# Optimization experiments

Hardware: AMD Instinct MI355X
Metric: run time of the kernel (lower is better)

Reference implementation:

```python
import jax, jax.numpy as jnp
import numpy as np

TOP_K = 10  # hard-coded k=10 in the original tf.nn.top_k call


def setup_inputs() -> dict:
    key = jax.random.key(0)
    k1, k2 = jax.random.split(key)
    x = jax.random.normal(k1, (32768, 128), dtype=jnp.float32)
    cluster_centers = jax.random.normal(k2, (512, 128), dtype=jnp.float32)
    return {"x": x, "cluster_centers": cluster_centers}


def reference(x, cluster_centers):
    # (mathematically identical to tf.norm(x[:, None, :] - centers, axis=-1)
    #  without materializing the [N, K, D] difference tensor).
    x2 = jnp.sum(x * x, axis=-1, keepdims=True)            # [N, 1]
    c2 = jnp.sum(cluster_centers * cluster_centers, -1)    # [K]
    d2 = x2 - 2.0 * (x @ cluster_centers.T) + c2           # [N, K]
    distances = jnp.sqrt(jnp.maximum(d2, 0.0))
    # top-k smallest distances -> cluster indices (values in [0, K))
    _, indices = jax.lax.top_k(-distances, TOP_K)          # [N, 10] int32
    # Faithful to the original: gather POINTS x at these cluster indices
    closest_points = x[indices]                            # [N, 10, D]
    return closest_points.reshape(1, -1, x.shape[-1])      # [1, N*10, D]
```

## Files before the change

kernel.cpp:

```cpp
#include <hip/hip_runtime.h>
#include <stdint.h>

#define NPTS 32768
#define NCEN 512
#define DIM  128
#define TOPK 10

#define BM 128
#define BN 128
#define LDT 132

__global__ __launch_bounds__(256) void np_rownorm(const float* __restrict__ src,
                                                  float* __restrict__ dst, int nrows) {
  const int t = threadIdx.x;
  const int lane = t & 63;
  const int wv = t >> 6;
  const int g = lane >> 3;
  const int j = lane & 7;
  const int row = blockIdx.x * 32 + wv * 8 + g;
  if (row >= nrows) return;
  const float* p = src + (size_t)row * DIM;

  float v = p[j];
  float r = __fmul_rn(v, v);
#pragma unroll
  for (int b = 1; b < 16; ++b) {
    v = p[8 * b + j];
    r = __fadd_rn(r, __fmul_rn(v, v));
  }
  r = __fadd_rn(r, __shfl_xor(r, 1, 64));
  r = __fadd_rn(r, __shfl_xor(r, 2, 64));
  r = __fadd_rn(r, __shfl_xor(r, 4, 64));
  if (j == 0) dst[row] = r;
}

__global__ __launch_bounds__(256) void dist_kernel(const float* __restrict__ x,
                                                   const float* __restrict__ cen,
                                                   const float* __restrict__ x2,
                                                   const float* __restrict__ c2,
                                                   float* __restrict__ dist) {
  __shared__ float xT[DIM][LDT];
  __shared__ float cT[DIM][LDT];

  const int t  = threadIdx.x;
  const int pb = blockIdx.y * BM;
  const int cb = blockIdx.x * BN;

  {
    const int p  = t & 127;
    const int kb = (t >> 7) * 64;
    const float4* srcx = (const float4*)&x[(size_t)(pb + p) * DIM + kb];
    const float4* srcc = (const float4*)&cen[(size_t)(cb + p) * DIM + kb];
#pragma unroll
    for (int i = 0; i < 16; ++i) {
      float4 v = srcx[i];
      int k = kb + i * 4;
      xT[k + 0][p] = v.x; xT[k + 1][p] = v.y; xT[k + 2][p] = v.z; xT[k + 3][p] = v.w;
    }
#pragma unroll
    for (int i = 0; i < 16; ++i) {
      float4 v = srcc[i];
      int k = kb + i * 4;
      cT[k + 0][p] = v.x; cT[k + 1][p] = v.y; cT[k + 2][p] = v.z; cT[k + 3][p] = v.w;
    }
  }
  __syncthreads();

  const int wid  = t >> 6;
  const int lane = t & 63;
  const int wr = wid >> 1, wc = wid & 1;
  const int r = lane & 7, c = lane >> 3;
  const int px = wr * 64 + 4 * r;
  const int cx = wc * 64 + 4 * c;

  float acc[8][8];
#pragma unroll
  for (int i = 0; i < 8; ++i)
#pragma unroll
    for (int j = 0; j < 8; ++j) acc[i][j] = 0.f;

#pragma unroll 4
  for (int k = 0; k < DIM; ++k) {
    float4 xa = *(const float4*)&xT[k][px];
    float4 xb = *(const float4*)&xT[k][px + 32];
    float4 ca = *(const float4*)&cT[k][cx];
    float4 cbv = *(const float4*)&cT[k][cx + 32];
    float xv[8] = {xa.x, xa.y, xa.z, xa.w, xb.x, xb.y, xb.z, xb.w};
    float cv[8] = {ca.x, ca.y, ca.z, ca.w, cbv.x, cbv.y, cbv.z, cbv.w};
#pragma unroll
    for (int i = 0; i < 8; ++i)
#pragma unroll
      for (int j = 0; j < 8; ++j)
        acc[i][j] = __fmaf_rn(xv[i], cv[j], acc[i][j]);
  }

#pragma unroll
  for (int i = 0; i < 8; ++i) {
    const int pt = px + (i & 3) + (i >> 2) * 32;
    const int p  = pb + pt;
    const float xx = x2[p];
#pragma unroll
    for (int jq = 0; jq < 2; ++jq) {
      const int cg = cb + cx + jq * 32;
      float4 cc = *(const float4*)&c2[cg];
      float t0 = __fmaf_rn(-2.f, acc[i][jq * 4 + 0], xx);
      float t1 = __fmaf_rn(-2.f, acc[i][jq * 4 + 1], xx);
      float t2 = __fmaf_rn(-2.f, acc[i][jq * 4 + 2], xx);
      float t3 = __fmaf_rn(-2.f, acc[i][jq * 4 + 3], xx);
      float4 o;
      o.x = sqrtf(fmaxf(__fadd_rn(t0, cc.x), 0.f));
      o.y = sqrtf(fmaxf(__fadd_rn(t1, cc.y), 0.f));
      o.z = sqrtf(fmaxf(__fadd_rn(t2, cc.z), 0.f));
      o.w = sqrtf(fmaxf(__fadd_rn(t3, cc.w), 0.f));
      *(float4*)&dist[(size_t)p * NCEN + cg] = o;
    }
  }
}

__global__ __launch_bounds__(256) void topk_gather_kernel(const float* __restrict__ dist,
                                                          const float* __restrict__ x,
                                                          float* __restrict__ out) {
  const int p    = blockIdx.x * 4 + (threadIdx.x >> 6);
  const int lane = threadIdx.x & 63;

  const float4* dp = (const float4*)(dist + (size_t)p * NCEN);
  float4 va = dp[lane];
  float4 vb = dp[lane + 64];

  unsigned long long key[8];
  {
    const unsigned ca = 4u * lane, cb = 256u + 4u * lane;
    key[0] = ((unsigned long long)__float_as_uint(va.x) << 32) | (ca + 0);
    key[1] = ((unsigned long long)__float_as_uint(va.y) << 32) | (ca + 1);
    key[2] = ((unsigned long long)__float_as_uint(va.z) << 32) | (ca + 2);
    key[3] = ((unsigned long long)__float_as_uint(va.w) << 32) | (ca + 3);
    key[4] = ((unsigned long long)__float_as_uint(vb.x) << 32) | (cb + 0);
    key[5] = ((unsigned long long)__float_as_uint(vb.y) << 32) | (cb + 1);
    key[6] = ((unsigned long long)__float_as_uint(vb.z) << 32) | (cb + 2);
    key[7] = ((unsigned long long)__float_as_uint(vb.w) << 32) | (cb + 3);
  }

  float* op = out + (size_t)p * TOPK * DIM;

#pragma unroll
  for (int t = 0; t < TOPK; ++t) {
    unsigned long long m = key[0];
#pragma unroll
    for (int s = 1; s < 8; ++s) m = (key[s] < m) ? key[s] : m;
#pragma unroll
    for (int off = 32; off > 0; off >>= 1) {
      unsigned long long o = __shfl_xor(m, off, 64);
      m = (o < m) ? o : m;
    }
#pragma unroll
    for (int s = 0; s < 8; ++s)
      if (key[s] == m) key[s] = ~0ull;

    const int idx = (int)(m & 0x1ffull);
    float2 v = *(const float2*)&x[(size_t)idx * DIM + 2 * lane];
    *(float2*)&op[(size_t)t * DIM + 2 * lane] = v;
  }
}

extern "C" void kernel_launch(void* const* d_in, const int* in_sizes, int n_in,
                              void* d_out, int out_size, void* d_ws, size_t ws_size,
                              hipStream_t stream) {
  const float* x   = (const float*)d_in[0];
  const float* cen = (const float*)d_in[1];
  float* out = (float*)d_out;

  float* c2   = (float*)d_ws;
  float* x2   = (float*)((char*)d_ws + 4096);
  float* dist = (float*)((char*)d_ws + 4096 + 131072);

  np_rownorm<<<NCEN / 32, 256, 0, stream>>>(cen, c2, NCEN);
  np_rownorm<<<NPTS / 32, 256, 0, stream>>>(x, x2, NPTS);
  dist_kernel<<<dim3(NCEN / BN, NPTS / BM), 256, 0, stream>>>(x, cen, x2, c2, dist);
  topk_gather_kernel<<<NPTS / 4, 256, 0, stream>>>(dist, x, out);
}
```

Baseline: 143.3 us.

## Tile the K dimension of the distance GEMM to shrink shared memory

The distance kernel now walks the 128-wide feature dimension in chunks of 32 instead of staging the whole tile at once. This cuts shared memory per block from about 135KB to about 34KB, and a launch bound asking for 4 blocks per multiprocessor is added so more blocks can be resident. The cost is four load/sync phases per block with no double buffering. The launch bound also caps registers for the 64-element accumulator, which could cause spills.

```diff
diff --git a/kernel.cpp b/kernel.cpp
--- a/kernel.cpp
+++ b/kernel.cpp
@@ -8,6 +8,7 @@
 
 #define BM 128
 #define BN 128
+#define KSTEP 32
 #define LDT 132
 
 __global__ __launch_bounds__(256) void np_rownorm(const float* __restrict__ src,
@@ -34,37 +35,20 @@
   if (j == 0) dst[row] = r;
 }
 
-__global__ __launch_bounds__(256) void dist_kernel(const float* __restrict__ x,
-                                                   const float* __restrict__ cen,
-                                                   const float* __restrict__ x2,
-                                                   const float* __restrict__ c2,
-                                                   float* __restrict__ dist) {
-  __shared__ float xT[DIM][LDT];
-  __shared__ float cT[DIM][LDT];
+__global__ __launch_bounds__(256, 4) void dist_kernel(const float* __restrict__ x,
+                                                      const float* __restrict__ cen,
+                                                      const float* __restrict__ x2,
+                                                      const float* __restrict__ c2,
+                                                      float* __restrict__ dist) {
+  __shared__ float xT[KSTEP][LDT];
+  __shared__ float cT[KSTEP][LDT];
 
   const int t  = threadIdx.x;
   const int pb = blockIdx.y * BM;
   const int cb = blockIdx.x * BN;
 
-  {
-    const int p  = t & 127;
-    const int kb = (t >> 7) * 64;
-    const float4* srcx = (const float4*)&x[(size_t)(pb + p) * DIM + kb];
-    const float4* srcc = (const float4*)&cen[(size_t)(cb + p) * DIM + kb];
-#pragma unroll
-    for (int i = 0; i < 16; ++i) {
-      float4 v = srcx[i];
-      int k = kb + i * 4;
-      xT[k + 0][p] = v.x; xT[k + 1][p] = v.y; xT[k + 2][p] = v.z; xT[k + 3][p] = v.w;
-    }
-#pragma unroll
-    for (int i = 0; i < 16; ++i) {
-      float4 v = srcc[i];
-      int k = kb + i * 4;
-      cT[k + 0][p] = v.x; cT[k + 1][p] = v.y; cT[k + 2][p] = v.z; cT[k + 3][p] = v.w;
-    }
-  }
-  __syncthreads();
+  const int srow = t & 127;
+  const int kh   = (t >> 7) * 16;
 
   const int wid  = t >> 6;
   const int lane = t & 63;
@@ -79,19 +63,40 @@
 #pragma unroll
     for (int j = 0; j < 8; ++j) acc[i][j] = 0.f;
 
+  for (int s = 0; s < DIM / KSTEP; ++s) {
+    if (s) __syncthreads();
+    {
+      const float4* srcx = (const float4*)&x[(size_t)(pb + srow) * DIM + s * KSTEP + kh];
+      const float4* srcc = (const float4*)&cen[(size_t)(cb + srow) * DIM + s * KSTEP + kh];
+#pragma unroll
+      for (int i = 0; i < 4; ++i) {
+        float4 v = srcx[i];
+        int k = kh + i * 4;
+        xT[k + 0][srow] = v.x; xT[k + 1][srow] = v.y; xT[k + 2][srow] = v.z; xT[k + 3][srow] = v.w;
+      }
+#pragma unroll
+      for (int i = 0; i < 4; ++i) {
+        float4 v = srcc[i];
+        int k = kh + i * 4;
+        cT[k + 0][srow] = v.x; cT[k + 1][srow] = v.y; cT[k + 2][srow] = v.z; cT[k + 3][srow] = v.w;
+      }
+    }
+    __syncthreads();
+
 #pragma unroll 4
-  for (int k = 0; k < DIM; ++k) {
-    float4 xa = *(const float4*)&xT[k][px];
-    float4 xb = *(const float4*)&xT[k][px + 32];
-    float4 ca = *(const float4*)&cT[k][cx];
-    float4 cbv = *(const float4*)&cT[k][cx + 32];
-    float xv[8] = {xa.x, xa.y, xa.z, xa.w, xb.x, xb.y, xb.z, xb.w};
-    float cv[8] = {ca.x, ca.y, ca.z, ca.w, cbv.x, cbv.y, cbv.z, cbv.w};
+    for (int kk = 0; kk < KSTEP; ++kk) {
+      float4 xa  = *(const float4*)&xT[kk][px];
+      float4 xb  = *(const float4*)&xT[kk][px + 32];
+      float4 ca  = *(const float4*)&cT[kk][cx];
+      float4 cbv = *(const float4*)&cT[kk][cx + 32];
+      float xv[8] = {xa.x, xa.y, xa.z, xa.w, xb.x, xb.y, xb.z, xb.w};
+      float cv[8] = {ca.x, ca.y, ca.z, ca.w, cbv.x, cbv.y, cbv.z, cbv.w};
 #pragma unroll
-    for (int i = 0; i < 8; ++i)
+      for (int i = 0; i < 8; ++i)
 #pragma unroll
-      for (int j = 0; j < 8; ++j)
-        acc[i][j] = __fmaf_rn(xv[i], cv[j], acc[i][j]);
+        for (int j = 0; j < 8; ++j)
+          acc[i][j] = __fmaf_rn(xv[i], cv[j], acc[i][j]);
+    }
   }
 
 #pragma unroll
```

Result: faster. 123.6 us (-13.7%).
